# Kernel tuning notes

Measured on AMD Instinct MI355X. Metric: run time of the kernel, lower is better.

The kernel has to match this reference:

```python
import jax, jax.numpy as jnp
import numpy as np

TEMPERATURE = 2.0  # exp(log(2.0)) clamped to [0.1, 10] -> 2.0
EPS = 1e-8
B, D, P = 2048, 256, 4


def setup_inputs() -> dict:
    key = jax.random.key(0)
    k1, k2, k3, k4 = jax.random.split(key, 4)
    return {
        'z_i': jax.random.normal(k1, (B, D), dtype=jnp.float32),
        'z_j': jax.random.normal(k2, (B, D), dtype=jnp.float32),
        'physics_i': jax.random.uniform(k3, (B, P), dtype=jnp.float32),
        'physics_j': jax.random.uniform(k4, (B, P), dtype=jnp.float32),
    }


def _offdiag(x, flat_idx, n):
    # extract off-diagonal entries of (n,n) -> (n, n-1), row-major order
    return jnp.take(x.reshape(-1), flat_idx).reshape(n, n - 1)


def reference(z_i, z_j, physics_i, physics_j):
    features = jnp.concatenate([z_i, z_j], axis=0)          # (n, D)
    labels = jnp.concatenate([physics_i, physics_j], axis=0)  # (n, P)
    n = features.shape[0]

    # pairwise L1 label distances (n, n)
    label_diffs = jnp.abs(labels[:, None, :] - labels[None, :, :]).sum(-1)

    # cosine similarity logits (n, n)
    f = features / jnp.linalg.norm(features, axis=-1, keepdims=True)
    logits = (f @ f.T) / TEMPERATURE
    logits = logits - jax.lax.stop_gradient(jnp.max(logits, axis=1, keepdims=True))
    exp_logits = jnp.exp(logits)

    flat_idx = jnp.asarray(np.flatnonzero(~np.eye(n, dtype=bool)))
    logits_o = _offdiag(logits, flat_idx, n)      # (n, n-1)
    exp_o = _offdiag(exp_logits, flat_idx, n)
    ld_o = _offdiag(label_diffs, flat_idx, n)

    # denom[i,k] = sum_j [ld_o[i,j] >= ld_o[i,k]] * exp_o[i,j]
    # computed via per-row sort + cumsum instead of the O(n^3) mask loop
    order = jnp.argsort(ld_o, axis=1)
    ld_sorted = jnp.take_along_axis(ld_o, order, axis=1)
    exp_sorted = jnp.take_along_axis(exp_o, order, axis=1)
    csum = jnp.cumsum(exp_sorted, axis=1)
    total = csum[:, -1:]
    # rank[i,k] = number of j with ld_o[i,j] < ld_o[i,k]  (side='left' handles ties)
    rank = jax.vmap(lambda s, q: jnp.searchsorted(s, q, side='left'))(ld_sorted, ld_o)
    below = jnp.where(rank > 0,
                      jnp.take_along_axis(csum, jnp.maximum(rank - 1, 0), axis=1),
                      0.0)
    denom = total - below                          # (n, n-1)

    pos_log_probs = logits_o - jnp.log(denom + EPS)
    loss = -pos_log_probs.sum() / (n * (n - 1))
    return loss
```

## Files before the change

kernel.cpp:

```cpp
#include <hip/hip_runtime.h>
#include <float.h>
#include <math.h>

#define B_SZ   2048
#define D_DIM  256
#define P_DIM  4
#define N_TOT  4096
#define EPS_F  1e-8f
#define RPP    16
#define NBK    512
#define BSCALE 128.0f
#define FIXS   1048576.0f

typedef short  s16x8 __attribute__((ext_vector_type(8)));
typedef float  f32x4 __attribute__((ext_vector_type(4)));

__device__ __forceinline__ unsigned short f2bf(float x) {
    unsigned int b = __float_as_uint(x);
    b += 0x7FFFu + ((b >> 16) & 1u);
    return (unsigned short)(b >> 16);
}

__global__ __launch_bounds__(64) void normalize_kernel(
    const float* __restrict__ z_i, const float* __restrict__ z_j,
    unsigned short* __restrict__ fb)
{
    int row  = blockIdx.x;
    int lane = threadIdx.x;
    const float* src = (row < B_SZ) ? (z_i + (size_t)row * D_DIM)
                                    : (z_j + (size_t)(row - B_SZ) * D_DIM);
    float4 v = ((const float4*)src)[lane];
    float ss = v.x*v.x + v.y*v.y + v.z*v.z + v.w*v.w;
    #pragma unroll
    for (int off = 32; off > 0; off >>= 1)
        ss += __shfl_down(ss, off, 64);
    ss = __shfl(ss, 0, 64);
    float inv = 1.0f / sqrtf(ss);
    ushort4 o;
    o.x = f2bf(v.x * inv); o.y = f2bf(v.y * inv);
    o.z = f2bf(v.z * inv); o.w = f2bf(v.w * inv);
    ((ushort4*)(fb + (size_t)row * D_DIM))[lane] = o;
}

__global__ __launch_bounds__(512, 2) void panel_kernel(
    const unsigned short* __restrict__ fb,
    const float* __restrict__ physics_i, const float* __restrict__ physics_j,
    float* __restrict__ partial)
{
    __shared__ unsigned long long hist[RPP * NBK];
    __shared__ float scr[8];

    int tid = threadIdx.x;
    int L   = tid & 63;
    int w   = tid >> 6;
    int i0  = blockIdx.x * RPP;

    uint4 zu = {0u, 0u, 0u, 0u};
    #pragma unroll
    for (int t = 0; t < 8; ++t)
        ((uint4*)hist)[tid + t * 512] = zu;

    uint4 a4[8];
    #pragma unroll
    for (int kc = 0; kc < 8; ++kc)
        a4[kc] = *(const uint4*)(fb + (size_t)(i0 + (L & 15)) * D_DIM
                                 + kc * 32 + (L >> 4) * 8);
    float4 Lr[4];
    #pragma unroll
    for (int q = 0; q < 4; ++q) {
        int r = i0 + (L >> 4) * 4 + q;
        const float* p = (r < B_SZ) ? physics_i + (size_t)r * P_DIM
                                    : physics_j + (size_t)(r - B_SZ) * P_DIM;
        Lr[q] = *(const float4*)p;
    }

    __syncthreads();

    #define LOADB(BB, LJ, ct)                                                     \
        {                                                                         \
            int jc_ = (ct) * 128 + w * 16 + (L & 15);                             \
            const unsigned short* bp_ = fb + (size_t)jc_ * D_DIM + (L >> 4) * 8;  \
            _Pragma("unroll")                                                     \
            for (int kc = 0; kc < 8; ++kc)                                        \
                BB[kc] = *(const s16x8*)(bp_ + kc * 32);                          \
            const float* pj_ = (jc_ < B_SZ)                                       \
                ? physics_i + (size_t)jc_ * P_DIM                                 \
                : physics_j + (size_t)(jc_ - B_SZ) * P_DIM;                       \
            LJ = *(const float4*)pj_;                                             \
        }

    #define COMPUTE(BB, LJ, ct)                                                   \
        {                                                                         \
            int jc_ = (ct) * 128 + w * 16 + (L & 15);                             \
            f32x4 acc0 = {0.f, 0.f, 0.f, 0.f};                                    \
            f32x4 acc1 = {0.f, 0.f, 0.f, 0.f};                                    \
            _Pragma("unroll")                                                     \
            for (int kc = 0; kc < 4; ++kc) {                                      \
                acc0 = __builtin_amdgcn_mfma_f32_16x16x32_bf16(                   \
                    __builtin_bit_cast(s16x8, a4[2*kc]),   BB[2*kc],   acc0, 0, 0, 0); \
                acc1 = __builtin_amdgcn_mfma_f32_16x16x32_bf16(                   \
                    __builtin_bit_cast(s16x8, a4[2*kc+1]), BB[2*kc+1], acc1, 0, 0, 0); \
            }                                                                     \
            _Pragma("unroll")                                                     \
            for (int q = 0; q < 4; ++q) {                                         \
                int rq = (L >> 4) * 4 + q;                                        \
                float logit = (acc0[q] + acc1[q]) * 0.5f;              \
                float d = fabsf(Lr[q].x - LJ.x) + fabsf(Lr[q].y - LJ.y)           \
                        + fabsf(Lr[q].z - LJ.z) + fabsf(Lr[q].w - LJ.w);          \
                int bk = (int)(d * BSCALE); if (bk > NBK - 1) bk = NBK - 1;       \
                if (jc_ != i0 + rq) {                                             \
                    unsigned long long upd = (1ULL << 40)                         \
                        + (unsigned long long)(__expf(logit) * FIXS);             \
                    atomicAdd(&hist[rq * NBK + bk], upd);                         \
                    SL += logit;                                                  \
                }                                                                 \
            }                                                                     \
        }

    float SL = 0.f;
    s16x8  bA[8], bB[8];
    float4 LjA, LjB;
    LOADB(bA, LjA, 0)
    for (int ct = 0; ct < 32; ct += 2) {
        LOADB(bB, LjB, ct + 1)
        COMPUTE(bA, LjA, ct)
        if (ct + 2 < 32) LOADB(bA, LjA, ct + 2)
        COMPUTE(bB, LjB, ct + 1)
    }
    __syncthreads();

    float term = 0.f;
    #pragma unroll
    for (int rr = 0; rr < 2; ++rr) {
        int row = w * 2 + rr;
        const unsigned long long* hr = hist + row * NBK + L * 8;
        float    v[8];
        unsigned c[8];
        float fs = 0.f;
        #pragma unroll
        for (int k = 0; k < 8; ++k) {
            unsigned long long x = hr[k];
            v[k] = (float)(x & 0xFFFFFFFFFFULL) * (1.0f / FIXS);
            c[k] = (unsigned)(x >> 40);
            fs += v[k];
        }
        float s = fs;
        #pragma unroll
        for (int off = 1; off < 64; off <<= 1) {
            float u = __shfl_down(s, off, 64);
            if (L + off < 64) s += u;
        }
        float run = s - fs;
        #pragma unroll
        for (int k = 7; k >= 0; --k) {
            run += v[k];
            if (c[k]) term += (float)c[k] * __logf(run + EPS_F);
        }
    }

    float acc = SL - term;
    #pragma unroll
    for (int off = 32; off > 0; off >>= 1)
        acc += __shfl_down(acc, off, 64);
    if (L == 0) scr[w] = acc;
    __syncthreads();
    if (tid == 0) {
        float s = 0.f;
        #pragma unroll
        for (int w2 = 0; w2 < 8; ++w2) s += scr[w2];
        partial[blockIdx.x] = s;
    }
    #undef LOADB
    #undef COMPUTE
}

__global__ __launch_bounds__(256) void final_kernel(
    const float* __restrict__ partial, float* __restrict__ out)
{
    __shared__ float red[4];
    int tid = threadIdx.x;
    float s = 0.f;
    for (int i = tid; i < N_TOT / RPP; i += 256) s += partial[i];
    #pragma unroll
    for (int off = 32; off > 0; off >>= 1)
        s += __shfl_down(s, off, 64);
    if ((tid & 63) == 0) red[tid >> 6] = s;
    __syncthreads();
    if (tid == 0) {
        double tot = (double)red[0] + red[1] + red[2] + red[3];
        out[0] = (float)(-tot / ((double)N_TOT * (N_TOT - 1)));
    }
}

extern "C" void kernel_launch(void* const* d_in, const int* in_sizes, int n_in,
                              void* d_out, int out_size, void* d_ws, size_t ws_size,
                              hipStream_t stream)
{
    const float* z_i  = (const float*)d_in[0];
    const float* z_j  = (const float*)d_in[1];
    const float* ph_i = (const float*)d_in[2];
    const float* ph_j = (const float*)d_in[3];

    unsigned short* fb      = (unsigned short*)d_ws;
    float*          partial = (float*)(fb + (size_t)N_TOT * D_DIM);

    normalize_kernel<<<N_TOT, 64, 0, stream>>>(z_i, z_j, fb);
    panel_kernel<<<N_TOT / RPP, 512, 0, stream>>>(fb, ph_i, ph_j, partial);
    final_kernel<<<1, 256, 0, stream>>>(partial, (float*)d_out);
}
```

Baseline: 130.5 us.

## Quantize normalized features to FP8 and use fp8 MFMA with 1024-thread panels

Normalized features are now packed to FP8 instead of bf16, and the similarity GEMM uses the fp8 MFMA instruction with 8-byte operands. This halves the feature load traffic and the register footprint of the operands. The panel block also doubles to 1024 threads, so each wave covers half as many column tiles and handles one histogram row in the epilogue. FP8 lowers the accuracy of the logits, which feed exp and log terms, so the loss may drift from the reference.

```diff
diff --git a/kernel.cpp b/kernel.cpp
--- a/kernel.cpp
+++ b/kernel.cpp
@@ -12,18 +12,12 @@
 #define BSCALE 128.0f
 #define FIXS   1048576.0f
 
-typedef short  s16x8 __attribute__((ext_vector_type(8)));
-typedef float  f32x4 __attribute__((ext_vector_type(4)));
-
-__device__ __forceinline__ unsigned short f2bf(float x) {
-    unsigned int b = __float_as_uint(x);
-    b += 0x7FFFu + ((b >> 16) & 1u);
-    return (unsigned short)(b >> 16);
-}
+typedef float     f32x4 __attribute__((ext_vector_type(4)));
+typedef long long i64;
 
 __global__ __launch_bounds__(64) void normalize_kernel(
     const float* __restrict__ z_i, const float* __restrict__ z_j,
-    unsigned short* __restrict__ fb)
+    unsigned char* __restrict__ fbq)
 {
     int row  = blockIdx.x;
     int lane = threadIdx.x;
@@ -36,19 +30,18 @@
         ss += __shfl_down(ss, off, 64);
     ss = __shfl(ss, 0, 64);
     float inv = 1.0f / sqrtf(ss);
-    ushort4 o;
-    o.x = f2bf(v.x * inv); o.y = f2bf(v.y * inv);
-    o.z = f2bf(v.z * inv); o.w = f2bf(v.w * inv);
-    ((ushort4*)(fb + (size_t)row * D_DIM))[lane] = o;
-}
-
-__global__ __launch_bounds__(512, 2) void panel_kernel(
-    const unsigned short* __restrict__ fb,
+    int p = __builtin_amdgcn_cvt_pk_fp8_f32(v.x * inv, v.y * inv, 0, false);
+    p     = __builtin_amdgcn_cvt_pk_fp8_f32(v.z * inv, v.w * inv, p, true);
+    ((int*)(fbq + (size_t)row * D_DIM))[lane] = p;
+}
+
+__global__ __launch_bounds__(1024, 4) void panel_kernel(
+    const unsigned char* __restrict__ fbq,
     const float* __restrict__ physics_i, const float* __restrict__ physics_j,
     float* __restrict__ partial)
 {
     __shared__ unsigned long long hist[RPP * NBK];
-    __shared__ float scr[8];
+    __shared__ float scr[16];
 
     int tid = threadIdx.x;
     int L   = tid & 63;
@@ -57,14 +50,16 @@
 
     uint4 zu = {0u, 0u, 0u, 0u};
     #pragma unroll
-    for (int t = 0; t < 8; ++t)
-        ((uint4*)hist)[tid + t * 512] = zu;
-
-    uint4 a4[8];
-    #pragma unroll
-    for (int kc = 0; kc < 8; ++kc)
-        a4[kc] = *(const uint4*)(fb + (size_t)(i0 + (L & 15)) * D_DIM
-                                 + kc * 32 + (L >> 4) * 8);
+    for (int t = 0; t < 4; ++t)
+        ((uint4*)hist)[tid + t * 1024] = zu;
+
+    i64 a8[8];
+    {
+        const unsigned char* ap = fbq + (size_t)(i0 + (L & 15)) * D_DIM + (L >> 4) * 8;
+        #pragma unroll
+        for (int kc = 0; kc < 8; ++kc)
+            a8[kc] = *(const i64*)(ap + kc * 32);
+    }
     float4 Lr[4];
     #pragma unroll
     for (int q = 0; q < 4; ++q) {
@@ -78,11 +73,11 @@
 
     #define LOADB(BB, LJ, ct)                                                     \
         {                                                                         \
-            int jc_ = (ct) * 128 + w * 16 + (L & 15);                             \
-            const unsigned short* bp_ = fb + (size_t)jc_ * D_DIM + (L >> 4) * 8;  \
+            int jc_ = (ct) * 256 + w * 16 + (L & 15);                             \
+            const unsigned char* bp_ = fbq + (size_t)jc_ * D_DIM + (L >> 4) * 8;  \
             _Pragma("unroll")                                                     \
             for (int kc = 0; kc < 8; ++kc)                                        \
-                BB[kc] = *(const s16x8*)(bp_ + kc * 32);                          \
+                BB[kc] = *(const i64*)(bp_ + kc * 32);                            \
             const float* pj_ = (jc_ < B_SZ)                                       \
                 ? physics_i + (size_t)jc_ * P_DIM                                 \
                 : physics_j + (size_t)(jc_ - B_SZ) * P_DIM;                       \
@@ -91,15 +86,15 @@
 
     #define COMPUTE(BB, LJ, ct)                                                   \
         {                                                                         \
-            int jc_ = (ct) * 128 + w * 16 + (L & 15);                             \
+            int jc_ = (ct) * 256 + w * 16 + (L & 15);                             \
             f32x4 acc0 = {0.f, 0.f, 0.f, 0.f};                                    \
             f32x4 acc1 = {0.f, 0.f, 0.f, 0.f};                                    \
             _Pragma("unroll")                                                     \
             for (int kc = 0; kc < 4; ++kc) {                                      \
-                acc0 = __builtin_amdgcn_mfma_f32_16x16x32_bf16(                   \
-                    __builtin_bit_cast(s16x8, a4[2*kc]),   BB[2*kc],   acc0, 0, 0, 0); \
-                acc1 = __builtin_amdgcn_mfma_f32_16x16x32_bf16(                   \
-                    __builtin_bit_cast(s16x8, a4[2*kc+1]), BB[2*kc+1], acc1, 0, 0, 0); \
+                acc0 = __builtin_amdgcn_mfma_f32_16x16x32_fp8_fp8(                \
+                    a8[2*kc],   BB[2*kc],   acc0, 0, 0, 0);                       \
+                acc1 = __builtin_amdgcn_mfma_f32_16x16x32_fp8_fp8(                \
+                    a8[2*kc+1], BB[2*kc+1], acc1, 0, 0, 0);                       \
             }                                                                     \
             _Pragma("unroll")                                                     \
             for (int q = 0; q < 4; ++q) {                                         \
@@ -118,22 +113,20 @@
         }
 
     float SL = 0.f;
-    s16x8  bA[8], bB[8];
+    i64    bA[8], bB[8];
     float4 LjA, LjB;
     LOADB(bA, LjA, 0)
-    for (int ct = 0; ct < 32; ct += 2) {
+    for (int ct = 0; ct < 16; ct += 2) {
         LOADB(bB, LjB, ct + 1)
         COMPUTE(bA, LjA, ct)
-        if (ct + 2 < 32) LOADB(bA, LjA, ct + 2)
+        if (ct + 2 < 16) LOADB(bA, LjA, ct + 2)
         COMPUTE(bB, LjB, ct + 1)
     }
     __syncthreads();
 
     float term = 0.f;
-    #pragma unroll
-    for (int rr = 0; rr < 2; ++rr) {
-        int row = w * 2 + rr;
-        const unsigned long long* hr = hist + row * NBK + L * 8;
+    {
+        const unsigned long long* hr = hist + w * NBK + L * 8;
         float    v[8];
         unsigned c[8];
         float fs = 0.f;
@@ -167,7 +160,7 @@
     if (tid == 0) {
         float s = 0.f;
         #pragma unroll
-        for (int w2 = 0; w2 < 8; ++w2) s += scr[w2];
+        for (int w2 = 0; w2 < 16; ++w2) s += scr[w2];
         partial[blockIdx.x] = s;
     }
     #undef LOADB
@@ -201,10 +194,10 @@
     const float* ph_i = (const float*)d_in[2];
     const float* ph_j = (const float*)d_in[3];
 
-    unsigned short* fb      = (unsigned short*)d_ws;
-    float*          partial = (float*)(fb + (size_t)N_TOT * D_DIM);
-
-    normalize_kernel<<<N_TOT, 64, 0, stream>>>(z_i, z_j, fb);
-    panel_kernel<<<N_TOT / RPP, 512, 0, stream>>>(fb, ph_i, ph_j, partial);
+    unsigned char* fbq     = (unsigned char*)d_ws;
+    float*         partial = (float*)(fbq + (size_t)N_TOT * D_DIM);
+
+    normalize_kernel<<<N_TOT, 64, 0, stream>>>(z_i, z_j, fbq);
+    panel_kernel<<<N_TOT / RPP, 1024, 0, stream>>>(fbq, ph_i, ph_j, partial);
     final_kernel<<<1, 256, 0, stream>>>(partial, (float*)d_out);
 }
```

New measurement: 129.1 us, median of 2. About the same (-1.1%).
